# Kernel tuning notes

Hardware: AMD Instinct MI355X
Metric: run time of the kernel (lower is better)

## Reference

```python
import jax, jax.numpy as jnp
import numpy as np

N_BLADES = 8  # Cl(3,0): 1, e1, e2, e3 and their products (bitmask blade indexing)


def _blade_sign(a: int, b: int) -> int:
    # Sign from reordering basis vectors when multiplying blades a*b (Euclidean metric).
    a >>= 1
    s = 0
    while a:
        s += bin(a & b).count('1')
        a >>= 1
    return -1 if (s & 1) else 1


def make_cayley() -> np.ndarray:
    C = np.zeros((N_BLADES, N_BLADES, N_BLADES), dtype=np.float32)
    for a in range(N_BLADES):
        for b in range(N_BLADES):
            C[a, b, a ^ b] = float(_blade_sign(a, b))
    return C


def setup_inputs() -> dict:
    key = jax.random.key(0)
    k1, k2 = jax.random.split(key)
    B, Cin, Cout = 8192, 256, 256
    scale = 1.0 / np.sqrt(Cin * N_BLADES)
    x = jax.random.normal(k1, (B, Cin, N_BLADES), dtype=jnp.float32)
    weight = jax.random.normal(k2, (Cout, Cin, N_BLADES), dtype=jnp.float32) * scale
    bias = jnp.zeros((Cout, N_BLADES), dtype=jnp.float32)
    cayley = jnp.asarray(make_cayley())
    return {"x": x, "weight": weight, "bias": bias, "cayley": cayley}


def reference(x, weight, bias, cayley):
    # A[b,o,j,k] = sum_i W[o,i,j] * X[b,i,k]  (weight blade j times input blade k)
    A = jnp.einsum('oij,bik->bojk', weight, x)
    # Contract blade pair (j,k) into output blade l via sparse Cayley table.
    out = jnp.einsum('jkl,bojk->bol', cayley, A)
    return out + bias[None, :, :]
```

## Files before the change

kernel.cpp:

```cpp
#include <hip/hip_runtime.h>
#include <stdint.h>
#include <stddef.h>


typedef __bf16 bf16x8  __attribute__((ext_vector_type(8)));
typedef float  f32x4   __attribute__((ext_vector_type(4)));

#define BM 256
#define BN 256
#define KSLICE 32
#define NSLICES 64
#define SLOT_ELEMS (256 * 32)

__device__ __forceinline__ void async_copy16(void* lds_dst, const void* g_src) {
    __builtin_amdgcn_global_load_lds(
        (__attribute__((address_space(1))) void*)g_src,
        (__attribute__((address_space(3))) void*)lds_dst,
        16, 0, 0);
}

__global__ __launch_bounds__(256) void prep_kernel(
    const float* __restrict__ x, __bf16* __restrict__ Xb, long nx,
    const float* __restrict__ W, const float* __restrict__ cayley,
    __bf16* __restrict__ Wt, int Cin, int Cout, int castBlocks)
{
    __shared__ float Cay[512];
    if ((int)blockIdx.x < castBlocks) {
        long i = ((long)blockIdx.x * 256 + threadIdx.x) * 8;
        if (i + 8 <= nx) {
            const f32x4* p = (const f32x4*)(x + i);
            f32x4 v0 = p[0];
            f32x4 v1 = p[1];
            bf16x8 o;
            o[0] = (__bf16)v0[0]; o[1] = (__bf16)v0[1];
            o[2] = (__bf16)v0[2]; o[3] = (__bf16)v0[3];
            o[4] = (__bf16)v1[0]; o[5] = (__bf16)v1[1];
            o[6] = (__bf16)v1[2]; o[7] = (__bf16)v1[3];
            *(bf16x8*)(Xb + i) = o;
        }
        return;
    }
    for (int t = threadIdx.x; t < 512; t += 256) Cay[t] = cayley[t];
    __syncthreads();

    int flat = (blockIdx.x - castBlocks) * 256 + threadIdx.x;
    int total = Cout * 8 * Cin;
    if (flat >= total) return;
    int i = flat % Cin;
    int n = flat / Cin;
    int o = n >> 3, l = n & 7;

    const float* wrow = W + ((size_t)o * Cin + i) * 8;
    float w8[8];
    #pragma unroll
    for (int j = 0; j < 8; ++j) w8[j] = wrow[j];

    bf16x8 outv;
    #pragma unroll
    for (int k = 0; k < 8; ++k) {
        float s = 0.f;
        #pragma unroll
        for (int j = 0; j < 8; ++j) s += Cay[j * 64 + k * 8 + l] * w8[j];
        outv[k] = (__bf16)s;
    }
    *(bf16x8*)(Wt + (size_t)n * (Cin * 8) + i * 8) = outv;
}

__global__ __launch_bounds__(512, 2) void gemm_bt_kernel(
    const __bf16* __restrict__ A,
    const __bf16* __restrict__ Bt,
    const float*  __restrict__ bias,
    float* __restrict__ C,
    int M, int N, int K)
{
    __shared__ __align__(16) __bf16 As[4][SLOT_ELEMS];
    __shared__ __align__(16) __bf16 Bs[4][SLOT_ELEMS];

    const int tid  = threadIdx.x;
    const int wave = tid >> 6;
    const int lane = tid & 63;
    const int quad = lane >> 4;
    const int l16  = lane & 15;

    const int bid = blockIdx.x;
    const int xcd = bid & 7;
    const int idx = bid >> 3;
    const int mBase = (xcd * 4 + (idx & 3)) * BM;
    const int nBase = (idx >> 2) * BN;

    const int srow = lane >> 2;
    const int sgrp = (lane & 3) ^ ((lane >> 3) & 3);
    const __bf16* gA0 = A  + (size_t)(mBase + wave * 32 +  0 + srow) * K + sgrp * 8;
    const __bf16* gA1 = A  + (size_t)(mBase + wave * 32 + 16 + srow) * K + sgrp * 8;
    const __bf16* gB0 = Bt + (size_t)(nBase + wave * 32 +  0 + srow) * K + sgrp * 8;
    const __bf16* gB1 = Bt + (size_t)(nBase + wave * 32 + 16 + srow) * K + sgrp * 8;
    const int stOff = wave * 1024;

#define STAGE_A(slot, q) do {                                             \
        async_copy16(&As[slot][stOff      ], gA0 + (size_t)(q) * KSLICE); \
        async_copy16(&As[slot][stOff + 512], gA1 + (size_t)(q) * KSLICE); \
    } while (0)
#define STAGE_B(slot, q) do {                                             \
        async_copy16(&Bs[slot][stOff      ], gB0 + (size_t)(q) * KSLICE); \
        async_copy16(&Bs[slot][stOff + 512], gB1 + (size_t)(q) * KSLICE); \
    } while (0)

    const int wm = wave >> 2;
    const int wn = wave & 3;
    const int offq = (quad ^ ((l16 >> 1) & 3)) * 8;
    const __bf16* paBase = &As[0][(wm * 128 + l16) * KSLICE + offq];
    const __bf16* pbBase = &Bs[0][(wn * 64  + l16) * KSLICE + offq];

    f32x4 acc[8][4] = {};
    bf16x8 af0A[4], bfA[4], af0B[4], bfB[4], af1[4];

    STAGE_A(0, 0); STAGE_B(0, 0);
    STAGE_A(1, 1); STAGE_B(1, 1);
    STAGE_A(2, 2); STAGE_B(2, 2);
    STAGE_B(3, 3);
    asm volatile("s_waitcnt vmcnt(10)" ::: "memory");
    __builtin_amdgcn_s_barrier();

    #pragma unroll
    for (int j = 0; j < 4; ++j)
        af0A[j] = *(const bf16x8*)(paBase + j * 512);
    #pragma unroll
    for (int j = 0; j < 4; ++j)
        bfA[j]  = *(const bf16x8*)(pbBase + j * 512);

#define SLICE_BODY(s_, c_, n_, AF0, BF, NAF0, NBF, DOA, DOB, DOPF)             \
    do {                                                                       \
        _Pragma("unroll")                                                      \
        for (int j = 0; j < 4; ++j)                                            \
            af1[j] = *(const bf16x8*)(paBase + (c_) * SLOT_ELEMS + (4 + j) * 512); \
        if (DOA) STAGE_A(((s_) + 3) & 3, (s_) + 3);                            \
        __builtin_amdgcn_s_setprio(1);                                         \
        _Pragma("unroll")                                                      \
        for (int j = 0; j < 4; ++j)                                            \
            _Pragma("unroll")                                                  \
            for (int n = 0; n < 4; ++n)                                        \
                acc[j][n] = __builtin_amdgcn_mfma_f32_16x16x32_bf16(           \
                    AF0[j], BF[n], acc[j][n], 0, 0, 0);                        \
        __builtin_amdgcn_s_setprio(0);                                         \
        asm volatile("s_waitcnt vmcnt(8)" ::: "memory");                       \
        __builtin_amdgcn_s_barrier();                                          \
        if (DOPF) {                                                            \
            _Pragma("unroll")                                                  \
            for (int j = 0; j < 4; ++j)                                        \
                NAF0[j] = *(const bf16x8*)(paBase + (n_) * SLOT_ELEMS + j * 512); \
            _Pragma("unroll")                                                  \
            for (int j = 0; j < 4; ++j)                                        \
                NBF[j] = *(const bf16x8*)(pbBase + (n_) * SLOT_ELEMS + j * 512); \
        }                                                                      \
        if (DOB) STAGE_B((s_) & 3, (s_) + 4);                                  \
        __builtin_amdgcn_s_setprio(1);                                         \
        _Pragma("unroll")                                                      \
        for (int j = 0; j < 4; ++j)                                            \
            _Pragma("unroll")                                                  \
            for (int n = 0; n < 4; ++n)                                        \
                acc[4 + j][n] = __builtin_amdgcn_mfma_f32_16x16x32_bf16(       \
                    af1[j], BF[n], acc[4 + j][n], 0, 0, 0);                    \
        __builtin_amdgcn_s_setprio(0);                                         \
        __builtin_amdgcn_s_barrier();                                          \
    } while (0)

    #pragma unroll 1
    for (int s4 = 0; s4 < 15; ++s4) {
        const int s = s4 * 4;
        SLICE_BODY(s + 0, 0, 1, af0A, bfA, af0B, bfB, true, true, true);
        SLICE_BODY(s + 1, 1, 2, af0B, bfB, af0A, bfA, true, true, true);
        SLICE_BODY(s + 2, 2, 3, af0A, bfA, af0B, bfB, true, true, true);
        SLICE_BODY(s + 3, 3, 0, af0B, bfB, af0A, bfA, true, true, true);
    }
    SLICE_BODY(60, 0, 1, af0A, bfA, af0B, bfB, true,  false, true);
    SLICE_BODY(61, 1, 2, af0B, bfB, af0A, bfA, false, false, true);
    SLICE_BODY(62, 2, 3, af0A, bfA, af0B, bfB, false, false, true);
    SLICE_BODY(63, 3, 0, af0B, bfB, af0A, bfA, false, false, false);
    asm volatile("s_waitcnt vmcnt(0)" ::: "memory");

#undef SLICE_BODY
#undef STAGE_A
#undef STAGE_B

    float bv[4];
    #pragma unroll
    for (int n = 0; n < 4; ++n)
        bv[n] = bias[nBase + wn * 64 + n * 16 + l16];

    #pragma unroll
    for (int m = 0; m < 8; ++m) {
        #pragma unroll
        for (int n = 0; n < 4; ++n) {
            const int col = nBase + wn * 64 + n * 16 + l16;
            #pragma unroll
            for (int r = 0; r < 4; ++r) {
                const int row = mBase + wm * 128 + m * 16 + quad * 4 + r;
                C[(size_t)row * N + col] = acc[m][n][r] + bv[n];
            }
        }
    }
}

extern "C" void kernel_launch(void* const* d_in, const int* in_sizes, int n_in,
                              void* d_out, int out_size, void* d_ws, size_t ws_size,
                              hipStream_t stream) {
    const float* x      = (const float*)d_in[0];
    const float* weight = (const float*)d_in[1];
    const float* bias   = (const float*)d_in[2];
    const float* cayley = (const float*)d_in[3];
    float* out = (float*)d_out;

    const int Cout = in_sizes[2] / 8;
    const int Cin  = in_sizes[1] / (Cout * 8);
    const int Bm   = in_sizes[0] / (Cin * 8);
    const int M = Bm;
    const int N = Cout * 8;
    const int K = Cin * 8;

    __bf16* Xb = (__bf16*)d_ws;
    __bf16* Wt = (__bf16*)((char*)d_ws + (size_t)M * K * 2);

    long nx = (long)M * K;
    int castBlocks = (int)(nx / 8 / 256);
    int foldBlocks = (N * Cin + 255) / 256;
    prep_kernel<<<castBlocks + foldBlocks, 256, 0, stream>>>(
        x, Xb, nx, weight, cayley, Wt, Cin, Cout, castBlocks);

    int grid = (M / BM) * (N / BN);
    gemm_bt_kernel<<<grid, 512, 0, stream>>>(Xb, Wt, bias, out, M, N, K);
}
```

Baseline: 176.4 us.

## Fuse fp32-to-bf16 input cast into GEMM A-tile staging via registers

Removes the separate cast pass over x (64 MB fp32 read plus 32 MB bf16 write and reread). The GEMM now loads fp32 x tiles into registers, converts them to bf16 and writes them into LDS, while the weight tile keeps using async global-to-LDS copies. The pipeline is restructured into a register double buffer (aE/aO) with new vmcnt and lgkmcnt waits, and A fragments are now read from LDS in each half-slice instead of being prefetched. In exchange, every tile block rereads fp32 x across the 16 N tiles, doubling A traffic, and it uses more VGPRs and VALU conversion work inside the main loop.

```diff
diff --git a/kernel.cpp b/kernel.cpp
--- a/kernel.cpp
+++ b/kernel.cpp
@@ -3,14 +3,13 @@
 #include <stddef.h>
 
 
-typedef __bf16 bf16x8  __attribute__((ext_vector_type(8)));
-typedef float  f32x4   __attribute__((ext_vector_type(4)));
+typedef __bf16 bf16x8 __attribute__((ext_vector_type(8)));
+typedef float  f32x4  __attribute__((ext_vector_type(4)));
 
 #define BM 256
 #define BN 256
 #define KSLICE 32
-#define NSLICES 64
-#define SLOT_ELEMS (256 * 32)
+#define SLOT 8192
 
 __device__ __forceinline__ void async_copy16(void* lds_dst, const void* g_src) {
     __builtin_amdgcn_global_load_lds(
@@ -19,31 +18,24 @@
         16, 0, 0);
 }
 
-__global__ __launch_bounds__(256) void prep_kernel(
-    const float* __restrict__ x, __bf16* __restrict__ Xb, long nx,
+__device__ __forceinline__ bf16x8 cvt2(f32x4 a, f32x4 b) {
+    bf16x8 r;
+    r[0] = (__bf16)a[0]; r[1] = (__bf16)a[1];
+    r[2] = (__bf16)a[2]; r[3] = (__bf16)a[3];
+    r[4] = (__bf16)b[0]; r[5] = (__bf16)b[1];
+    r[6] = (__bf16)b[2]; r[7] = (__bf16)b[3];
+    return r;
+}
+
+__global__ __launch_bounds__(256) void fold_kernel(
     const float* __restrict__ W, const float* __restrict__ cayley,
-    __bf16* __restrict__ Wt, int Cin, int Cout, int castBlocks)
+    __bf16* __restrict__ Wt, int Cin, int Cout)
 {
     __shared__ float Cay[512];
-    if ((int)blockIdx.x < castBlocks) {
-        long i = ((long)blockIdx.x * 256 + threadIdx.x) * 8;
-        if (i + 8 <= nx) {
-            const f32x4* p = (const f32x4*)(x + i);
-            f32x4 v0 = p[0];
-            f32x4 v1 = p[1];
-            bf16x8 o;
-            o[0] = (__bf16)v0[0]; o[1] = (__bf16)v0[1];
-            o[2] = (__bf16)v0[2]; o[3] = (__bf16)v0[3];
-            o[4] = (__bf16)v1[0]; o[5] = (__bf16)v1[1];
-            o[6] = (__bf16)v1[2]; o[7] = (__bf16)v1[3];
-            *(bf16x8*)(Xb + i) = o;
-        }
-        return;
-    }
     for (int t = threadIdx.x; t < 512; t += 256) Cay[t] = cayley[t];
     __syncthreads();
 
-    int flat = (blockIdx.x - castBlocks) * 256 + threadIdx.x;
+    int flat = blockIdx.x * 256 + threadIdx.x;
     int total = Cout * 8 * Cin;
     if (flat >= total) return;
     int i = flat % Cin;
@@ -67,14 +59,14 @@
 }
 
 __global__ __launch_bounds__(512, 2) void gemm_bt_kernel(
-    const __bf16* __restrict__ A,
+    const float*  __restrict__ X,
     const __bf16* __restrict__ Bt,
     const float*  __restrict__ bias,
     float* __restrict__ C,
     int M, int N, int K)
 {
-    __shared__ __align__(16) __bf16 As[4][SLOT_ELEMS];
-    __shared__ __align__(16) __bf16 Bs[4][SLOT_ELEMS];
+    __shared__ __align__(16) __bf16 As[4][SLOT];
+    __shared__ __align__(16) __bf16 Bs[4][SLOT];
 
     const int tid  = threadIdx.x;
     const int wave = tid >> 6;
@@ -90,19 +82,27 @@
 
     const int srow = lane >> 2;
     const int sgrp = (lane & 3) ^ ((lane >> 3) & 3);
-    const __bf16* gA0 = A  + (size_t)(mBase + wave * 32 +  0 + srow) * K + sgrp * 8;
-    const __bf16* gA1 = A  + (size_t)(mBase + wave * 32 + 16 + srow) * K + sgrp * 8;
+    const float* gXc0 = X + (size_t)(mBase + wave * 32 +  0 + srow) * K + sgrp * 8;
+    const float* gXc1 = X + (size_t)(mBase + wave * 32 + 16 + srow) * K + sgrp * 8;
     const __bf16* gB0 = Bt + (size_t)(nBase + wave * 32 +  0 + srow) * K + sgrp * 8;
     const __bf16* gB1 = Bt + (size_t)(nBase + wave * 32 + 16 + srow) * K + sgrp * 8;
     const int stOff = wave * 1024;
-
-#define STAGE_A(slot, q) do {                                             \
-        async_copy16(&As[slot][stOff      ], gA0 + (size_t)(q) * KSLICE); \
-        async_copy16(&As[slot][stOff + 512], gA1 + (size_t)(q) * KSLICE); \
-    } while (0)
-#define STAGE_B(slot, q) do {                                             \
-        async_copy16(&Bs[slot][stOff      ], gB0 + (size_t)(q) * KSLICE); \
-        async_copy16(&Bs[slot][stOff + 512], gB1 + (size_t)(q) * KSLICE); \
+    const int wdA0 = stOff + lane * 8;
+    const int wdA1 = stOff + 512 + lane * 8;
+
+#define ISSUE_A(SET, q) do {                                       \
+        SET[0] = *(const f32x4*)(gXc0 + (size_t)(q) * KSLICE);     \
+        SET[1] = *(const f32x4*)(gXc0 + (size_t)(q) * KSLICE + 4); \
+        SET[2] = *(const f32x4*)(gXc1 + (size_t)(q) * KSLICE);     \
+        SET[3] = *(const f32x4*)(gXc1 + (size_t)(q) * KSLICE + 4); \
+    } while (0)
+#define CVT_WRITE(SET, slot) do {                                  \
+        *(bf16x8*)&As[slot][wdA0] = cvt2(SET[0], SET[1]);          \
+        *(bf16x8*)&As[slot][wdA1] = cvt2(SET[2], SET[3]);          \
+    } while (0)
+#define STAGE_B(slot, q) do {                                              \
+        async_copy16(&Bs[slot][stOff      ], gB0 + (size_t)(q) * KSLICE);  \
+        async_copy16(&Bs[slot][stOff + 512], gB1 + (size_t)(q) * KSLICE);  \
     } while (0)
 
     const int wm = wave >> 2;
@@ -112,75 +112,82 @@
     const __bf16* pbBase = &Bs[0][(wn * 64  + l16) * KSLICE + offq];
 
     f32x4 acc[8][4] = {};
-    bf16x8 af0A[4], bfA[4], af0B[4], bfB[4], af1[4];
-
-    STAGE_A(0, 0); STAGE_B(0, 0);
-    STAGE_A(1, 1); STAGE_B(1, 1);
-    STAGE_A(2, 2); STAGE_B(2, 2);
-    STAGE_B(3, 3);
-    asm volatile("s_waitcnt vmcnt(10)" ::: "memory");
+    bf16x8 af0[4], af1[4], bfA[4], bfB[4];
+    f32x4 aE[4], aO[4];
+
+    ISSUE_A(aE, 0); ISSUE_A(aO, 1);
+    STAGE_B(0, 0);  STAGE_B(1, 1);
+    asm volatile("s_waitcnt vmcnt(8)" ::: "memory");
+    CVT_WRITE(aE, 0);
+    asm volatile("s_waitcnt vmcnt(4)" ::: "memory");
+    CVT_WRITE(aO, 1);
+    ISSUE_A(aO, 2);
+    STAGE_B(2, 2); STAGE_B(3, 3);
+    asm volatile("s_waitcnt vmcnt(8)" ::: "memory");
+    asm volatile("s_waitcnt lgkmcnt(0)" ::: "memory");
     __builtin_amdgcn_s_barrier();
-
-    #pragma unroll
-    for (int j = 0; j < 4; ++j)
-        af0A[j] = *(const bf16x8*)(paBase + j * 512);
-    #pragma unroll
-    for (int j = 0; j < 4; ++j)
-        bfA[j]  = *(const bf16x8*)(pbBase + j * 512);
-
-#define SLICE_BODY(s_, c_, n_, AF0, BF, NAF0, NBF, DOA, DOB, DOPF)             \
+    #pragma unroll
+    for (int n = 0; n < 4; ++n)
+        bfA[n] = *(const bf16x8*)(pbBase + n * 512);
+
+#define SLICE(s_, SC, SN, BF, NBF, AIS, ACV, DOA, DOB, DOCVT, DOPF, VM)        \
     do {                                                                       \
         _Pragma("unroll")                                                      \
-        for (int j = 0; j < 4; ++j)                                            \
-            af1[j] = *(const bf16x8*)(paBase + (c_) * SLOT_ELEMS + (4 + j) * 512); \
-        if (DOA) STAGE_A(((s_) + 3) & 3, (s_) + 3);                            \
+        for (int m = 0; m < 4; ++m)                                            \
+            af0[m] = *(const bf16x8*)(paBase + (SC) * SLOT + m * 512);         \
+        if (DOA) ISSUE_A(AIS, (s_) + 3);                                       \
         __builtin_amdgcn_s_setprio(1);                                         \
         _Pragma("unroll")                                                      \
-        for (int j = 0; j < 4; ++j)                                            \
+        for (int m = 0; m < 4; ++m)                                            \
             _Pragma("unroll")                                                  \
             for (int n = 0; n < 4; ++n)                                        \
-                acc[j][n] = __builtin_amdgcn_mfma_f32_16x16x32_bf16(           \
-                    AF0[j], BF[n], acc[j][n], 0, 0, 0);                        \
+                acc[m][n] = __builtin_amdgcn_mfma_f32_16x16x32_bf16(           \
+                    af0[m], BF[n], acc[m][n], 0, 0, 0);                        \
         __builtin_amdgcn_s_setprio(0);                                         \
-        asm volatile("s_waitcnt vmcnt(8)" ::: "memory");                       \
-        __builtin_amdgcn_s_barrier();                                          \
+        if ((VM) == 0)      asm volatile("s_waitcnt vmcnt(6)" ::: "memory");   \
+        else if ((VM) == 1) asm volatile("s_waitcnt vmcnt(0)" ::: "memory");   \
+        if (DOB) STAGE_B((s_) & 3, (s_) + 4);                                  \
+        if (DOCVT) CVT_WRITE(ACV, ((s_) + 2) & 3);                             \
+        _Pragma("unroll")                                                      \
+        for (int m = 0; m < 4; ++m)                                            \
+            af1[m] = *(const bf16x8*)(paBase + (SC) * SLOT + 2048 + m * 512);  \
         if (DOPF) {                                                            \
             _Pragma("unroll")                                                  \
-            for (int j = 0; j < 4; ++j)                                        \
-                NAF0[j] = *(const bf16x8*)(paBase + (n_) * SLOT_ELEMS + j * 512); \
-            _Pragma("unroll")                                                  \
-            for (int j = 0; j < 4; ++j)                                        \
-                NBF[j] = *(const bf16x8*)(pbBase + (n_) * SLOT_ELEMS + j * 512); \
+            for (int n = 0; n < 4; ++n)                                        \
+                NBF[n] = *(const bf16x8*)(pbBase + (SN) * SLOT + n * 512);     \
         }                                                                      \
-        if (DOB) STAGE_B((s_) & 3, (s_) + 4);                                  \
         __builtin_amdgcn_s_setprio(1);                                         \
         _Pragma("unroll")                                                      \
-        for (int j = 0; j < 4; ++j)                                            \
+        for (int m = 0; m < 4; ++m)                                            \
             _Pragma("unroll")                                                  \
             for (int n = 0; n < 4; ++n)                                        \
-                acc[4 + j][n] = __builtin_amdgcn_mfma_f32_16x16x32_bf16(       \
-                    af1[j], BF[n], acc[4 + j][n], 0, 0, 0);                    \
+                acc[4 + m][n] = __builtin_amdgcn_mfma_f32_16x16x32_bf16(       \
+                    af1[m], BF[n], acc[4 + m][n], 0, 0, 0);                    \
         __builtin_amdgcn_s_setprio(0);                                         \
+        asm volatile("s_waitcnt lgkmcnt(0)" ::: "memory");                     \
         __builtin_amdgcn_s_barrier();                                          \
     } while (0)
 
     #pragma unroll 1
-    for (int s4 = 0; s4 < 15; ++s4) {
-        const int s = s4 * 4;
-        SLICE_BODY(s + 0, 0, 1, af0A, bfA, af0B, bfB, true, true, true);
-        SLICE_BODY(s + 1, 1, 2, af0B, bfB, af0A, bfA, true, true, true);
-        SLICE_BODY(s + 2, 2, 3, af0A, bfA, af0B, bfB, true, true, true);
-        SLICE_BODY(s + 3, 3, 0, af0B, bfB, af0A, bfA, true, true, true);
+    for (int t = 0; t < 14; ++t) {
+        SLICE(4 * t + 0, 0, 1, bfA, bfB, aE, aO, true, true, true, true, 0);
+        SLICE(4 * t + 1, 1, 2, bfB, bfA, aO, aE, true, true, true, true, 0);
+        SLICE(4 * t + 2, 2, 3, bfA, bfB, aE, aO, true, true, true, true, 0);
+        SLICE(4 * t + 3, 3, 0, bfB, bfA, aO, aE, true, true, true, true, 0);
     }
-    SLICE_BODY(60, 0, 1, af0A, bfA, af0B, bfB, true,  false, true);
-    SLICE_BODY(61, 1, 2, af0B, bfB, af0A, bfA, false, false, true);
-    SLICE_BODY(62, 2, 3, af0A, bfA, af0B, bfB, false, false, true);
-    SLICE_BODY(63, 3, 0, af0B, bfB, af0A, bfA, false, false, false);
-    asm volatile("s_waitcnt vmcnt(0)" ::: "memory");
-
-#undef SLICE_BODY
-#undef STAGE_A
+    SLICE(56, 0, 1, bfA, bfB, aE, aO, true,  true,  true,  true,  0);
+    SLICE(57, 1, 2, bfB, bfA, aO, aE, true,  true,  true,  true,  0);
+    SLICE(58, 2, 3, bfA, bfB, aE, aO, true,  true,  true,  true,  0);
+    SLICE(59, 3, 0, bfB, bfA, aO, aE, true,  true,  true,  true,  0);
+    SLICE(60, 0, 1, bfA, bfB, aE, aO, true,  false, true,  true,  0);
+    SLICE(61, 1, 2, bfB, bfA, aO, aE, false, false, true,  true,  1);
+    SLICE(62, 2, 3, bfA, bfB, aE, aO, false, false, false, true,  2);
+    SLICE(63, 3, 0, bfB, bfA, aO, aE, false, false, false, false, 2);
+
+#undef SLICE
 #undef STAGE_B
+#undef CVT_WRITE
+#undef ISSUE_A
 
     float bv[4];
     #pragma unroll
@@ -217,15 +224,11 @@
     const int N = Cout * 8;
     const int K = Cin * 8;
 
-    __bf16* Xb = (__bf16*)d_ws;
-    __bf16* Wt = (__bf16*)((char*)d_ws + (size_t)M * K * 2);
-
-    long nx = (long)M * K;
-    int castBlocks = (int)(nx / 8 / 256);
+    __bf16* Wt = (__bf16*)d_ws;
+
     int foldBlocks = (N * Cin + 255) / 256;
-    prep_kernel<<<castBlocks + foldBlocks, 256, 0, stream>>>(
-        x, Xb, nx, weight, cayley, Wt, Cin, Cout, castBlocks);
+    fold_kernel<<<foldBlocks, 256, 0, stream>>>(weight, cayley, Wt, Cin, Cout);
 
     int grid = (M / BM) * (N / BN);
-    gemm_bt_kernel<<<grid, 512, 0, stream>>>(Xb, Wt, bias, out, M, N, K);
-}
+    gemm_bt_kernel<<<grid, 512, 0, stream>>>(x, Wt, bias, out, M, N, K);
+}
```

After: 192.0 us. 8.9% more time.
